# Kernel optimization log

Hardware: AMD Instinct MI355X
Metric: run time of the kernel (lower is better)

## Reference

```python
import jax, jax.numpy as jnp
import numpy as np

B, T, D = 16, 4096, 512
N_SLOTS = 64


def setup_inputs() -> dict:
    key = jax.random.key(0)
    ks = jax.random.split(key, 7)
    s = 1.0 / np.sqrt(D)  # keep tanh out of deep saturation, like orthogonal*0.9 init
    return {
        "x_seq": jax.random.normal(ks[0], (B, T, D), jnp.float32),
        "h_tape": jax.random.normal(ks[1], (B, N_SLOTS, D), jnp.float32) * 0.1,
        "h_work": jax.random.normal(ks[2], (B, D), jnp.float32) * 0.1,
        "W_h": jax.random.normal(ks[3], (D, D), jnp.float32) * s,
        "W_x": jax.random.normal(ks[4], (D, D), jnp.float32) * s,
        "b_h": jnp.zeros((D,), jnp.float32),
        "W_write": jax.random.normal(ks[5], (D, D), jnp.float32) * s,
    }


def reference(x_seq, h_tape, h_work, W_h, W_x, b_h, W_write):
    """Dual-memory Elman recurrence.

    Per step t:
      read_t  = softmax(h_tape @ h_work / sqrt(D)) @ h_tape   (content-based tape read)
      h_work  = tanh(W_h h_work + W_x x_t + read_t + b_h)
      tape write: slot (t mod n_slots) <- W_write h_work      (FIFO tape write)
    Returns (h_work_out [B,T,D], h_tape_final [B,S,D], last h_work [B,D]).
    """
    scale = jnp.asarray(1.0 / np.sqrt(D), x_seq.dtype)

    def step(carry, inp):
        tape, h = carry
        x_t, t = inp
        scores = jnp.einsum("bsd,bd->bs", tape, h) * scale        # [B,S]
        attn = jax.nn.softmax(scores, axis=-1)
        read = jnp.einsum("bs,bsd->bd", attn, tape)               # [B,D]
        h_new = jnp.tanh(h @ W_h.T + x_t @ W_x.T + read + b_h)    # [B,D]
        w_vec = h_new @ W_write.T                                 # [B,D]
        slot = t % N_SLOTS
        tape = jax.lax.dynamic_update_slice(tape, w_vec[:, None, :], (0, slot, 0))
        return (tape, h_new), h_new

    xs = (jnp.swapaxes(x_seq, 0, 1), jnp.arange(x_seq.shape[1]))
    (tape_f, _), h_seq = jax.lax.scan(step, (h_tape, h_work), xs)
    h_work_out = jnp.swapaxes(h_seq, 0, 1)  # [B,T,D]
    return h_work_out, tape_f, h_work_out[:, -1]
```

## Files before the change

kernel.cpp:

```cpp
#include <hip/hip_runtime.h>
#include <cstddef>

#define B_SZ   16
#define T_SZ   4096
#define D_SZ   512
#define NSLOT  64
#define NW     16
#define RPW    32
#define TP     36
#define SCALE  0.044194173824159216f

__device__ __align__(8) unsigned long long g_pb[B_SZ * NW * NSLOT];
__device__ __align__(8) unsigned long long g_hb[B_SZ * D_SZ];
__device__ __align__(8) unsigned long long g_q [B_SZ * NW];

#define AL(p)    __hip_atomic_load((p),  __ATOMIC_RELAXED, __HIP_MEMORY_SCOPE_AGENT)
#define AS(p,v)  __hip_atomic_store((p), (v), __ATOMIC_RELAXED, __HIP_MEMORY_SCOPE_AGENT)

__device__ __forceinline__ unsigned long long pk(float v, unsigned tag) {
    return ((unsigned long long)tag << 32) | (unsigned long long)__float_as_uint(v);
}
__device__ __forceinline__ float lo(unsigned long long v) {
    return __uint_as_float((unsigned)v);
}

__global__ __launch_bounds__(256)
void xw_gemm_kernel(const float* __restrict__ X, const float* __restrict__ Wx,
                    const float* __restrict__ bh, float* __restrict__ out)
{
    __shared__ float As[16][68];
    __shared__ float Bs[16][68];
    const int m0 = blockIdx.x * 64;
    const int n0 = blockIdx.y * 64;
    const int tid = threadIdx.x;
    const int tr = tid >> 4, tc = tid & 15;
    const int lrow = tid >> 2;
    const int lkk  = (tid & 3) * 4;

    float acc[4][4] = {};

    for (int k0 = 0; k0 < D_SZ; k0 += 16) {
        float4 av = *(const float4*)(X  + (size_t)(m0 + lrow) * D_SZ + k0 + lkk);
        float4 bv = *(const float4*)(Wx + (size_t)(n0 + lrow) * D_SZ + k0 + lkk);
        As[lkk+0][lrow] = av.x; As[lkk+1][lrow] = av.y;
        As[lkk+2][lrow] = av.z; As[lkk+3][lrow] = av.w;
        Bs[lkk+0][lrow] = bv.x; Bs[lkk+1][lrow] = bv.y;
        Bs[lkk+2][lrow] = bv.z; Bs[lkk+3][lrow] = bv.w;
        __syncthreads();
        #pragma unroll
        for (int kk = 0; kk < 16; ++kk) {
            float a[4], b[4];
            #pragma unroll
            for (int i = 0; i < 4; ++i) a[i] = As[kk][tr*4+i];
            #pragma unroll
            for (int j = 0; j < 4; ++j) b[j] = Bs[kk][tc*4+j];
            #pragma unroll
            for (int i = 0; i < 4; ++i)
                #pragma unroll
                for (int j = 0; j < 4; ++j)
                    acc[i][j] = fmaf(a[i], b[j], acc[i][j]);
        }
        __syncthreads();
    }
    #pragma unroll
    for (int i = 0; i < 4; ++i) {
        const int m = m0 + tr*4 + i;
        const int n = n0 + tc*4;
        float4 o;
        o.x = acc[i][0] + bh[n+0];
        o.y = acc[i][1] + bh[n+1];
        o.z = acc[i][2] + bh[n+2];
        o.w = acc[i][3] + bh[n+3];
        *(float4*)(out + (size_t)m * D_SZ + n) = o;
    }
}

__global__ __launch_bounds__(256, 1)
void recurrence_mw(const float* __restrict__ tape0, const float* __restrict__ h0,
                   const float* __restrict__ W_h, const float* __restrict__ W_w,
                   float* __restrict__ out)
{
    __shared__ __align__(16) float tp[NSLOT][TP];
    __shared__ __align__(16) float hh[D_SZ];
    __shared__ __align__(16) float hno[RPW];
    __shared__ float scr[NSLOT];
    __shared__ float es[NSLOT];
    __shared__ float zmv[RPW];
    __shared__ float rp8[8][RPW];
    __shared__ float sml[2];

    const int blk = blockIdx.x;
    const int xcd = blk & 7;
    const int jj0 = blk >> 3;
    const int b   = xcd * 2 + (jj0 & 1);
    const int w   = jj0 >> 1;
    const int R0  = w * RPW;
    const int tid = threadIdx.x;
    const int fb  = b * NW;
    const int g16 = tid >> 4, sj = tid & 15;
    const int sA  = tid >> 2, qA = tid & 3;
    const int sg  = tid >> 5, jB = tid & 31;

    if (tid < NSLOT) AS(&g_pb[((size_t)fb + w) * NSLOT + tid], 0ULL);
    if (tid < RPW)   AS(&g_hb[(size_t)b * D_SZ + R0 + tid], 0ULL);
    if (tid == 0)    AS(&g_q[fb + w], 0ULL);

    float4 wh0[8], wh1[8], ww0[8], ww1[8];
    {
        const float* a0 = W_h + (size_t)(R0 + g16)      * D_SZ + 4 * sj;
        const float* a1 = W_h + (size_t)(R0 + g16 + 16) * D_SZ + 4 * sj;
        const float* b0 = W_w + (size_t)(R0 + g16)      * D_SZ + 4 * sj;
        const float* b1 = W_w + (size_t)(R0 + g16 + 16) * D_SZ + 4 * sj;
        #pragma unroll
        for (int i = 0; i < 8; ++i) {
            wh0[i] = *(const float4*)(a0 + 64 * i);
            wh1[i] = *(const float4*)(a1 + 64 * i);
            ww0[i] = *(const float4*)(b0 + 64 * i);
            ww1[i] = *(const float4*)(b1 + 64 * i);
        }
    }

    for (int i = tid; i < NSLOT * RPW; i += 256) {
        const int s = i >> 5, j = i & 31;
        tp[s][j] = tape0[((size_t)b * NSLOT + s) * D_SZ + R0 + j];
    }
    for (int i = tid; i < D_SZ; i += 256) hh[i] = h0[(size_t)b * D_SZ + i];
    __syncthreads();

    float* outb = out + (size_t)b * T_SZ * D_SZ;

    if (tid < RPW) {
        hno[tid] = hh[R0 + tid];
        AS(&g_hb[(size_t)b * D_SZ + R0 + tid], pk(hh[R0 + tid], 1u));
    }
    __syncthreads();
    {
        const float* trow = &tp[sA][8 * qA];
        float4 t0 = *(const float4*)trow;
        float4 t1 = *(const float4*)(trow + 4);
        float4 h0v = *(const float4*)&hno[8 * qA];
        float4 h1v = *(const float4*)&hno[8 * qA + 4];
        float pp = t0.x*h0v.x + t0.y*h0v.y + t0.z*h0v.z + t0.w*h0v.w
                 + t1.x*h1v.x + t1.y*h1v.y + t1.z*h1v.z + t1.w*h1v.w;
        pp += __shfl_xor(pp, 1);
        pp += __shfl_xor(pp, 2);
        if (qA == 0) AS(&g_pb[((size_t)fb + w) * NSLOT + sA], pk(pp, 1u));
    }

    for (int t = 0; t < T_SZ; ++t) {
        const unsigned tgB = (unsigned)(t + 1);
        const int sp = (t - 1) & 63;

        float xwv = 0.f;
        if (tid < RPW) xwv = outb[(size_t)t * D_SZ + R0 + tid];
        {
            const unsigned long long* pb = &g_pb[((size_t)fb + qA * 4) * NSLOT + sA];
            const unsigned long long* hb = &g_hb[(size_t)b * D_SZ + 2 * tid];
            unsigned long long p0, p1, p2, p3, v0, v1;
            for (;;) {
                p0 = AL(pb);              p1 = AL(pb + NSLOT);
                p2 = AL(pb + 2 * NSLOT);  p3 = AL(pb + 3 * NSLOT);
                v0 = AL(hb);              v1 = AL(hb + 1);
                if ((unsigned)(p0 >> 32) == tgB && (unsigned)(p1 >> 32) == tgB &&
                    (unsigned)(p2 >> 32) == tgB && (unsigned)(p3 >> 32) == tgB &&
                    (unsigned)(v0 >> 32) == tgB && (unsigned)(v1 >> 32) == tgB) break;
                __builtin_amdgcn_s_sleep(1);
            }
            float s4 = lo(p0) + lo(p1) + lo(p2) + lo(p3);
            s4 += __shfl_xor(s4, 1);
            s4 += __shfl_xor(s4, 2);
            if (qA == 0) scr[sA] = s4 * SCALE;
            hh[2 * tid]     = lo(v0);
            hh[2 * tid + 1] = lo(v1);
        }
        __syncthreads();

        {
            float z0 = 0.f, z1 = 0.f, v0 = 0.f, v1 = 0.f;
            #pragma unroll
            for (int i = 0; i < 8; ++i) {
                float4 hr = *(const float4*)&hh[4 * sj + 64 * i];
                z0 = fmaf(wh0[i].x, hr.x, z0); z0 = fmaf(wh0[i].y, hr.y, z0);
                z0 = fmaf(wh0[i].z, hr.z, z0); z0 = fmaf(wh0[i].w, hr.w, z0);
                z1 = fmaf(wh1[i].x, hr.x, z1); z1 = fmaf(wh1[i].y, hr.y, z1);
                z1 = fmaf(wh1[i].z, hr.z, z1); z1 = fmaf(wh1[i].w, hr.w, z1);
                v0 = fmaf(ww0[i].x, hr.x, v0); v0 = fmaf(ww0[i].y, hr.y, v0);
                v0 = fmaf(ww0[i].z, hr.z, v0); v0 = fmaf(ww0[i].w, hr.w, v0);
                v1 = fmaf(ww1[i].x, hr.x, v1); v1 = fmaf(ww1[i].y, hr.y, v1);
                v1 = fmaf(ww1[i].z, hr.z, v1); v1 = fmaf(ww1[i].w, hr.w, v1);
            }
            #pragma unroll
            for (int o = 1; o <= 8; o <<= 1) {
                z0 += __shfl_xor(z0, o); z1 += __shfl_xor(z1, o);
                v0 += __shfl_xor(v0, o); v1 += __shfl_xor(v1, o);
            }
            if (sj == 0) {
                zmv[g16] = z0; zmv[g16 + 16] = z1;
                if (t > 0) { tp[sp][g16] = v0; tp[sp][g16 + 16] = v1; }
            }
        }
        __syncthreads();

        if (tid < 64) {
            const float v = (t > 0 && tid == sp) ? -3.0e38f : scr[tid];
            float m = v;
            #pragma unroll
            for (int o = 32; o; o >>= 1) m = fmaxf(m, __shfl_xor(m, o));
            const float e = __expf(v - m);
            float s = e;
            #pragma unroll
            for (int o = 32; o; o >>= 1) s += __shfl_xor(s, o);
            es[tid] = e;
            if (tid == 0) { sml[0] = m; sml[1] = s; }
        } else if (tid < 96 && t > 0) {
            const int ld = tid - 64;
            float qp = tp[sp][ld] * hh[R0 + ld];
            #pragma unroll
            for (int o = 1; o <= 16; o <<= 1) qp += __shfl_xor(qp, o);
            if (ld == 0) AS(&g_q[fb + w], pk(qp, tgB));
        }
        __syncthreads();

        {
            float acc = 0.f;
            #pragma unroll
            for (int s8 = 0; s8 < 8; ++s8)
                acc = fmaf(es[sg * 8 + s8], tp[sg * 8 + s8][jB], acc);
            rp8[sg][jB] = acc;
        }
        __syncthreads();

        if (tid < RPW) {
            const float rr = rp8[0][tid] + rp8[1][tid] + rp8[2][tid] + rp8[3][tid]
                           + rp8[4][tid] + rp8[5][tid] + rp8[6][tid] + rp8[7][tid];
            float rd;
            if (t > 0) {
                const unsigned long long* qp_ = &g_q[fb + (tid & 15)];
                unsigned long long qv;
                for (;;) {
                    qv = AL(qp_);
                    if ((unsigned)(qv >> 32) == tgB) break;
                    __builtin_amdgcn_s_sleep(1);
                }
                float qs = lo(qv);
                qs += __shfl_xor(qs, 1); qs += __shfl_xor(qs, 2);
                qs += __shfl_xor(qs, 4); qs += __shfl_xor(qs, 8);
                const float esig = __expf(qs * SCALE - sml[0]);
                rd = (rr + esig * tp[sp][tid]) / (sml[1] + esig);
            } else {
                rd = rr / sml[1];
            }
            const float hn = tanhf(zmv[tid] + rd + xwv);
            outb[(size_t)t * D_SZ + R0 + tid] = hn;
            AS(&g_hb[(size_t)b * D_SZ + R0 + tid], pk(hn, (unsigned)(t + 2)));
            hno[tid] = hn;
        }
        __syncthreads();

        {
            const float* trow = &tp[sA][8 * qA];
            float4 t0 = *(const float4*)trow;
            float4 t1 = *(const float4*)(trow + 4);
            float4 h0v = *(const float4*)&hno[8 * qA];
            float4 h1v = *(const float4*)&hno[8 * qA + 4];
            float pp = t0.x*h0v.x + t0.y*h0v.y + t0.z*h0v.z + t0.w*h0v.w
                     + t1.x*h1v.x + t1.y*h1v.y + t1.z*h1v.z + t1.w*h1v.w;
            pp += __shfl_xor(pp, 1);
            pp += __shfl_xor(pp, 2);
            if (qA == 0) AS(&g_pb[((size_t)fb + w) * NSLOT + sA], pk(pp, (unsigned)(t + 2)));
        }
    }

    {
        const unsigned long long* hb = &g_hb[(size_t)b * D_SZ + 2 * tid];
        unsigned long long v0, v1;
        const unsigned tgF = (unsigned)(T_SZ + 1);
        for (;;) {
            v0 = AL(hb); v1 = AL(hb + 1);
            if ((unsigned)(v0 >> 32) == tgF && (unsigned)(v1 >> 32) == tgF) break;
            __builtin_amdgcn_s_sleep(1);
        }
        hh[2 * tid]     = lo(v0);
        hh[2 * tid + 1] = lo(v1);
    }
    __syncthreads();
    {
        float v0 = 0.f, v1 = 0.f;
        #pragma unroll
        for (int i = 0; i < 8; ++i) {
            float4 hr = *(const float4*)&hh[4 * sj + 64 * i];
            v0 = fmaf(ww0[i].x, hr.x, v0); v0 = fmaf(ww0[i].y, hr.y, v0);
            v0 = fmaf(ww0[i].z, hr.z, v0); v0 = fmaf(ww0[i].w, hr.w, v0);
            v1 = fmaf(ww1[i].x, hr.x, v1); v1 = fmaf(ww1[i].y, hr.y, v1);
            v1 = fmaf(ww1[i].z, hr.z, v1); v1 = fmaf(ww1[i].w, hr.w, v1);
        }
        #pragma unroll
        for (int o = 1; o <= 8; o <<= 1) { v0 += __shfl_xor(v0, o); v1 += __shfl_xor(v1, o); }
        if (sj == 0) { tp[63][g16] = v0; tp[63][g16 + 16] = v1; }
    }
    __syncthreads();
    float* tout = out + (size_t)B_SZ * T_SZ * D_SZ + (size_t)b * NSLOT * D_SZ;
    for (int i = tid; i < NSLOT * RPW; i += 256) {
        const int s = i >> 5, j = i & 31;
        tout[(size_t)s * D_SZ + R0 + j] = tp[s][j];
    }
    if (w == 0) {
        float* lout = out + (size_t)B_SZ * T_SZ * D_SZ
                          + (size_t)B_SZ * NSLOT * D_SZ + (size_t)b * D_SZ;
        for (int i = tid; i < D_SZ; i += 256) lout[i] = hh[i];
    }
}

extern "C" void kernel_launch(void* const* d_in, const int* in_sizes, int n_in,
                              void* d_out, int out_size, void* d_ws, size_t ws_size,
                              hipStream_t stream)
{
    const float* x_seq   = (const float*)d_in[0];
    const float* h_tape  = (const float*)d_in[1];
    const float* h_work  = (const float*)d_in[2];
    const float* W_h     = (const float*)d_in[3];
    const float* W_x     = (const float*)d_in[4];
    const float* b_h     = (const float*)d_in[5];
    const float* W_write = (const float*)d_in[6];
    float* out = (float*)d_out;

    dim3 g1(T_SZ * B_SZ / 64, D_SZ / 64);
    xw_gemm_kernel<<<g1, 256, 0, stream>>>(x_seq, W_x, b_h, out);

    recurrence_mw<<<B_SZ * NW, 256, 0, stream>>>(h_tape, h_work, W_h, W_write, out);
}
```

Measured before the change: 18.40 ms.

## Interleave four batch chains per workgroup to hide cross-block sync latency

```diff
diff --git a/kernel.cpp b/kernel.cpp
--- a/kernel.cpp
+++ b/kernel.cpp
@@ -7,12 +7,12 @@
 #define NSLOT  64
 #define NW     16
 #define RPW    32
+#define NC     4
 #define TP     36
 #define SCALE  0.044194173824159216f
 
 __device__ __align__(8) unsigned long long g_pb[B_SZ * NW * NSLOT];
 __device__ __align__(8) unsigned long long g_hb[B_SZ * D_SZ];
-__device__ __align__(8) unsigned long long g_q [B_SZ * NW];
 
 #define AL(p)    __hip_atomic_load((p),  __ATOMIC_RELAXED, __HIP_MEMORY_SCOPE_AGENT)
 #define AS(p,v)  __hip_atomic_store((p), (v), __ATOMIC_RELAXED, __HIP_MEMORY_SCOPE_AGENT)
@@ -23,6 +23,8 @@
 __device__ __forceinline__ float lo(unsigned long long v) {
     return __uint_as_float((unsigned)v);
 }
+#define PIN(x) asm volatile("" : "+v"(x))
+#define PIN4(v) do { PIN((v).x); PIN((v).y); PIN((v).z); PIN((v).w); } while (0)
 
 __global__ __launch_bounds__(256)
 void xw_gemm_kernel(const float* __restrict__ X, const float* __restrict__ Wx,
@@ -80,30 +82,30 @@
                    const float* __restrict__ W_h, const float* __restrict__ W_w,
                    float* __restrict__ out)
 {
-    __shared__ __align__(16) float tp[NSLOT][TP];
-    __shared__ __align__(16) float hh[D_SZ];
-    __shared__ __align__(16) float hno[RPW];
-    __shared__ float scr[NSLOT];
-    __shared__ float es[NSLOT];
-    __shared__ float zmv[RPW];
-    __shared__ float rp8[8][RPW];
-    __shared__ float sml[2];
+    __shared__ __align__(16) float tp[NC][NSLOT][TP];
+    __shared__ __align__(16) float hh[NC][D_SZ];
+    __shared__ float scr[NC][NSLOT];
+    __shared__ float es[NC][NSLOT];
+    __shared__ float zmv[NC][RPW];
+    __shared__ float rp8[NC][8][RPW];
+    __shared__ float sml[NC];
+    __shared__ float xwc[NC][RPW];
 
     const int blk = blockIdx.x;
-    const int xcd = blk & 7;
-    const int jj0 = blk >> 3;
-    const int b   = xcd * 2 + (jj0 & 1);
-    const int w   = jj0 >> 1;
+    const int w   = blk & 15;
+    const int g   = blk >> 4;
     const int R0  = w * RPW;
     const int tid = threadIdx.x;
-    const int fb  = b * NW;
     const int g16 = tid >> 4, sj = tid & 15;
     const int sA  = tid >> 2, qA = tid & 3;
     const int sg  = tid >> 5, jB = tid & 31;
 
-    if (tid < NSLOT) AS(&g_pb[((size_t)fb + w) * NSLOT + tid], 0ULL);
-    if (tid < RPW)   AS(&g_hb[(size_t)b * D_SZ + R0 + tid], 0ULL);
-    if (tid == 0)    AS(&g_q[fb + w], 0ULL);
+    #pragma unroll
+    for (int c = 0; c < NC; ++c) {
+        const int b = g * NC + c;
+        if (tid < NSLOT) AS(&g_pb[((size_t)b * NW + w) * NSLOT + tid], 0ULL);
+        if (tid < RPW)   AS(&g_hb[(size_t)b * D_SZ + R0 + tid], 0ULL);
+    }
 
     float4 wh0[8], wh1[8], ww0[8], ww1[8];
     {
@@ -113,201 +115,186 @@
         const float* b1 = W_w + (size_t)(R0 + g16 + 16) * D_SZ + 4 * sj;
         #pragma unroll
         for (int i = 0; i < 8; ++i) {
-            wh0[i] = *(const float4*)(a0 + 64 * i);
-            wh1[i] = *(const float4*)(a1 + 64 * i);
-            ww0[i] = *(const float4*)(b0 + 64 * i);
-            ww1[i] = *(const float4*)(b1 + 64 * i);
-        }
-    }
-
-    for (int i = tid; i < NSLOT * RPW; i += 256) {
-        const int s = i >> 5, j = i & 31;
-        tp[s][j] = tape0[((size_t)b * NSLOT + s) * D_SZ + R0 + j];
-    }
-    for (int i = tid; i < D_SZ; i += 256) hh[i] = h0[(size_t)b * D_SZ + i];
+            wh0[i] = *(const float4*)(a0 + 64 * i);  PIN4(wh0[i]);
+            wh1[i] = *(const float4*)(a1 + 64 * i);  PIN4(wh1[i]);
+            ww0[i] = *(const float4*)(b0 + 64 * i);  PIN4(ww0[i]);
+            ww1[i] = *(const float4*)(b1 + 64 * i);  PIN4(ww1[i]);
+        }
+    }
+
+    for (int c = 0; c < NC; ++c) {
+        const int b = g * NC + c;
+        for (int i = tid; i < NSLOT * RPW; i += 256) {
+            const int s = i >> 5, j = i & 31;
+            tp[c][s][j] = tape0[((size_t)b * NSLOT + s) * D_SZ + R0 + j];
+        }
+        for (int i = tid; i < D_SZ; i += 256) hh[c][i] = h0[(size_t)b * D_SZ + i];
+    }
     __syncthreads();
 
-    float* outb = out + (size_t)b * T_SZ * D_SZ;
-
-    if (tid < RPW) {
-        hno[tid] = hh[R0 + tid];
-        AS(&g_hb[(size_t)b * D_SZ + R0 + tid], pk(hh[R0 + tid], 1u));
-    }
-    __syncthreads();
-    {
-        const float* trow = &tp[sA][8 * qA];
-        float4 t0 = *(const float4*)trow;
-        float4 t1 = *(const float4*)(trow + 4);
-        float4 h0v = *(const float4*)&hno[8 * qA];
-        float4 h1v = *(const float4*)&hno[8 * qA + 4];
-        float pp = t0.x*h0v.x + t0.y*h0v.y + t0.z*h0v.z + t0.w*h0v.w
-                 + t1.x*h1v.x + t1.y*h1v.y + t1.z*h1v.z + t1.w*h1v.w;
-        pp += __shfl_xor(pp, 1);
-        pp += __shfl_xor(pp, 2);
-        if (qA == 0) AS(&g_pb[((size_t)fb + w) * NSLOT + sA], pk(pp, 1u));
-    }
-
     for (int t = 0; t < T_SZ; ++t) {
-        const unsigned tgB = (unsigned)(t + 1);
+        const unsigned tgP = (unsigned)(t + 1);
         const int sp = (t - 1) & 63;
 
-        float xwv = 0.f;
-        if (tid < RPW) xwv = outb[(size_t)t * D_SZ + R0 + tid];
+        #pragma unroll 1
+        for (int c = 0; c < NC; ++c) {
+            const int b = g * NC + c;
+            float* ob = out + (size_t)b * T_SZ * D_SZ;
+            if (tid < RPW) xwc[c][tid] = ob[(size_t)t * D_SZ + R0 + tid];
+            if (t > 0) {
+                const unsigned long long* hb = &g_hb[(size_t)b * D_SZ + 2 * tid];
+                unsigned long long v0, v1;
+                for (;;) {
+                    v0 = AL(hb); v1 = AL(hb + 1);
+                    if ((unsigned)(v0 >> 32) == tgP && (unsigned)(v1 >> 32) == tgP) break;
+                    __builtin_amdgcn_s_sleep(1);
+                }
+                hh[c][2 * tid]     = lo(v0);
+                hh[c][2 * tid + 1] = lo(v1);
+            }
+            __syncthreads();
+
+            {
+                float z0 = 0.f, z1 = 0.f, y0 = 0.f, y1 = 0.f;
+                #pragma unroll
+                for (int i = 0; i < 8; ++i) {
+                    float4 hr = *(const float4*)&hh[c][4 * sj + 64 * i];
+                    z0 = fmaf(wh0[i].x, hr.x, z0); z0 = fmaf(wh0[i].y, hr.y, z0);
+                    z0 = fmaf(wh0[i].z, hr.z, z0); z0 = fmaf(wh0[i].w, hr.w, z0);
+                    z1 = fmaf(wh1[i].x, hr.x, z1); z1 = fmaf(wh1[i].y, hr.y, z1);
+                    z1 = fmaf(wh1[i].z, hr.z, z1); z1 = fmaf(wh1[i].w, hr.w, z1);
+                    y0 = fmaf(ww0[i].x, hr.x, y0); y0 = fmaf(ww0[i].y, hr.y, y0);
+                    y0 = fmaf(ww0[i].z, hr.z, y0); y0 = fmaf(ww0[i].w, hr.w, y0);
+                    y1 = fmaf(ww1[i].x, hr.x, y1); y1 = fmaf(ww1[i].y, hr.y, y1);
+                    y1 = fmaf(ww1[i].z, hr.z, y1); y1 = fmaf(ww1[i].w, hr.w, y1);
+                }
+                #pragma unroll
+                for (int o = 1; o <= 8; o <<= 1) {
+                    z0 += __shfl_xor(z0, o); z1 += __shfl_xor(z1, o);
+                    y0 += __shfl_xor(y0, o); y1 += __shfl_xor(y1, o);
+                }
+                if (sj == 0) {
+                    zmv[c][g16] = z0; zmv[c][g16 + 16] = z1;
+                    if (t > 0) { tp[c][sp][g16] = y0; tp[c][sp][g16 + 16] = y1; }
+                }
+            }
+            __syncthreads();
+
+            {
+                const float* trow = &tp[c][sA][8 * qA];
+                float4 t0 = *(const float4*)trow;
+                float4 t1 = *(const float4*)(trow + 4);
+                float4 ha = *(const float4*)&hh[c][R0 + 8 * qA];
+                float4 hb4 = *(const float4*)&hh[c][R0 + 8 * qA + 4];
+                float pp = t0.x*ha.x + t0.y*ha.y + t0.z*ha.z + t0.w*ha.w
+                         + t1.x*hb4.x + t1.y*hb4.y + t1.z*hb4.z + t1.w*hb4.w;
+                pp += __shfl_xor(pp, 1);
+                pp += __shfl_xor(pp, 2);
+                if (qA == 0)
+                    AS(&g_pb[((size_t)b * NW + w) * NSLOT + sA], pk(pp, tgP));
+            }
+        }
+
+        #pragma unroll 1
+        for (int c = 0; c < NC; ++c) {
+            const int b = g * NC + c;
+            float* ob = out + (size_t)b * T_SZ * D_SZ;
+            {
+                const unsigned long long* pb =
+                    &g_pb[((size_t)b * NW + qA * 4) * NSLOT + sA];
+                unsigned long long p0, p1, p2, p3;
+                for (;;) {
+                    p0 = AL(pb);             p1 = AL(pb + NSLOT);
+                    p2 = AL(pb + 2 * NSLOT); p3 = AL(pb + 3 * NSLOT);
+                    if ((unsigned)(p0 >> 32) == tgP && (unsigned)(p1 >> 32) == tgP &&
+                        (unsigned)(p2 >> 32) == tgP && (unsigned)(p3 >> 32) == tgP) break;
+                    __builtin_amdgcn_s_sleep(1);
+                }
+                float s4 = lo(p0) + lo(p1) + lo(p2) + lo(p3);
+                s4 += __shfl_xor(s4, 1);
+                s4 += __shfl_xor(s4, 2);
+                if (qA == 0) scr[c][sA] = s4 * SCALE;
+            }
+            __syncthreads();
+
+            if (tid < 64) {
+                const float v = scr[c][tid];
+                float m = v;
+                #pragma unroll
+                for (int o = 32; o; o >>= 1) m = fmaxf(m, __shfl_xor(m, o));
+                const float e = __expf(v - m);
+                float s = e;
+                #pragma unroll
+                for (int o = 32; o; o >>= 1) s += __shfl_xor(s, o);
+                es[c][tid] = e;
+                if (tid == 0) sml[c] = s;
+            }
+            __syncthreads();
+
+            {
+                float acc = 0.f;
+                #pragma unroll
+                for (int s8 = 0; s8 < 8; ++s8)
+                    acc = fmaf(es[c][sg * 8 + s8], tp[c][sg * 8 + s8][jB], acc);
+                rp8[c][sg][jB] = acc;
+            }
+            __syncthreads();
+
+            if (tid < RPW) {
+                const float rr = rp8[c][0][tid] + rp8[c][1][tid] + rp8[c][2][tid]
+                               + rp8[c][3][tid] + rp8[c][4][tid] + rp8[c][5][tid]
+                               + rp8[c][6][tid] + rp8[c][7][tid];
+                const float rd = rr / sml[c];
+                const float hn = tanhf(zmv[c][tid] + rd + xwc[c][tid]);
+                AS(&g_hb[(size_t)b * D_SZ + R0 + tid], pk(hn, (unsigned)(t + 2)));
+                ob[(size_t)t * D_SZ + R0 + tid] = hn;
+            }
+        }
+    }
+
+    for (int c = 0; c < NC; ++c) {
+        const int b = g * NC + c;
         {
-            const unsigned long long* pb = &g_pb[((size_t)fb + qA * 4) * NSLOT + sA];
             const unsigned long long* hb = &g_hb[(size_t)b * D_SZ + 2 * tid];
-            unsigned long long p0, p1, p2, p3, v0, v1;
+            const unsigned tgF = (unsigned)(T_SZ + 1);
+            unsigned long long v0, v1;
             for (;;) {
-                p0 = AL(pb);              p1 = AL(pb + NSLOT);
-                p2 = AL(pb + 2 * NSLOT);  p3 = AL(pb + 3 * NSLOT);
-                v0 = AL(hb);              v1 = AL(hb + 1);
-                if ((unsigned)(p0 >> 32) == tgB && (unsigned)(p1 >> 32) == tgB &&
-                    (unsigned)(p2 >> 32) == tgB && (unsigned)(p3 >> 32) == tgB &&
-                    (unsigned)(v0 >> 32) == tgB && (unsigned)(v1 >> 32) == tgB) break;
+                v0 = AL(hb); v1 = AL(hb + 1);
+                if ((unsigned)(v0 >> 32) == tgF && (unsigned)(v1 >> 32) == tgF) break;
                 __builtin_amdgcn_s_sleep(1);
             }
-            float s4 = lo(p0) + lo(p1) + lo(p2) + lo(p3);
-            s4 += __shfl_xor(s4, 1);
-            s4 += __shfl_xor(s4, 2);
-            if (qA == 0) scr[sA] = s4 * SCALE;
-            hh[2 * tid]     = lo(v0);
-            hh[2 * tid + 1] = lo(v1);
-        }
-        __syncthreads();
-
+            hh[c][2 * tid]     = lo(v0);
+            hh[c][2 * tid + 1] = lo(v1);
+        }
+        __syncthreads();
         {
-            float z0 = 0.f, z1 = 0.f, v0 = 0.f, v1 = 0.f;
+            float y0 = 0.f, y1 = 0.f;
             #pragma unroll
             for (int i = 0; i < 8; ++i) {
-                float4 hr = *(const float4*)&hh[4 * sj + 64 * i];
-                z0 = fmaf(wh0[i].x, hr.x, z0); z0 = fmaf(wh0[i].y, hr.y, z0);
-                z0 = fmaf(wh0[i].z, hr.z, z0); z0 = fmaf(wh0[i].w, hr.w, z0);
-                z1 = fmaf(wh1[i].x, hr.x, z1); z1 = fmaf(wh1[i].y, hr.y, z1);
-                z1 = fmaf(wh1[i].z, hr.z, z1); z1 = fmaf(wh1[i].w, hr.w, z1);
-                v0 = fmaf(ww0[i].x, hr.x, v0); v0 = fmaf(ww0[i].y, hr.y, v0);
-                v0 = fmaf(ww0[i].z, hr.z, v0); v0 = fmaf(ww0[i].w, hr.w, v0);
-                v1 = fmaf(ww1[i].x, hr.x, v1); v1 = fmaf(ww1[i].y, hr.y, v1);
-                v1 = fmaf(ww1[i].z, hr.z, v1); v1 = fmaf(ww1[i].w, hr.w, v1);
+                float4 hr = *(const float4*)&hh[c][4 * sj + 64 * i];
+                y0 = fmaf(ww0[i].x, hr.x, y0); y0 = fmaf(ww0[i].y, hr.y, y0);
+                y0 = fmaf(ww0[i].z, hr.z, y0); y0 = fmaf(ww0[i].w, hr.w, y0);
+                y1 = fmaf(ww1[i].x, hr.x, y1); y1 = fmaf(ww1[i].y, hr.y, y1);
+                y1 = fmaf(ww1[i].z, hr.z, y1); y1 = fmaf(ww1[i].w, hr.w, y1);
             }
             #pragma unroll
             for (int o = 1; o <= 8; o <<= 1) {
-                z0 += __shfl_xor(z0, o); z1 += __shfl_xor(z1, o);
-                v0 += __shfl_xor(v0, o); v1 += __shfl_xor(v1, o);
-            }
-            if (sj == 0) {
-                zmv[g16] = z0; zmv[g16 + 16] = z1;
-                if (t > 0) { tp[sp][g16] = v0; tp[sp][g16 + 16] = v1; }
-            }
-        }
-        __syncthreads();
-
-        if (tid < 64) {
-            const float v = (t > 0 && tid == sp) ? -3.0e38f : scr[tid];
-            float m = v;
-            #pragma unroll
-            for (int o = 32; o; o >>= 1) m = fmaxf(m, __shfl_xor(m, o));
-            const float e = __expf(v - m);
-            float s = e;
-            #pragma unroll
-            for (int o = 32; o; o >>= 1) s += __shfl_xor(s, o);
-            es[tid] = e;
-            if (tid == 0) { sml[0] = m; sml[1] = s; }
-        } else if (tid < 96 && t > 0) {
-            const int ld = tid - 64;
-            float qp = tp[sp][ld] * hh[R0 + ld];
-            #pragma unroll
-            for (int o = 1; o <= 16; o <<= 1) qp += __shfl_xor(qp, o);
-            if (ld == 0) AS(&g_q[fb + w], pk(qp, tgB));
-        }
-        __syncthreads();
-
-        {
-            float acc = 0.f;
-            #pragma unroll
-            for (int s8 = 0; s8 < 8; ++s8)
-                acc = fmaf(es[sg * 8 + s8], tp[sg * 8 + s8][jB], acc);
-            rp8[sg][jB] = acc;
-        }
-        __syncthreads();
-
-        if (tid < RPW) {
-            const float rr = rp8[0][tid] + rp8[1][tid] + rp8[2][tid] + rp8[3][tid]
-                           + rp8[4][tid] + rp8[5][tid] + rp8[6][tid] + rp8[7][tid];
-            float rd;
-            if (t > 0) {
-                const unsigned long long* qp_ = &g_q[fb + (tid & 15)];
-                unsigned long long qv;
-                for (;;) {
-                    qv = AL(qp_);
-                    if ((unsigned)(qv >> 32) == tgB) break;
-                    __builtin_amdgcn_s_sleep(1);
-                }
-                float qs = lo(qv);
-                qs += __shfl_xor(qs, 1); qs += __shfl_xor(qs, 2);
-                qs += __shfl_xor(qs, 4); qs += __shfl_xor(qs, 8);
-                const float esig = __expf(qs * SCALE - sml[0]);
-                rd = (rr + esig * tp[sp][tid]) / (sml[1] + esig);
-            } else {
-                rd = rr / sml[1];
-            }
-            const float hn = tanhf(zmv[tid] + rd + xwv);
-            outb[(size_t)t * D_SZ + R0 + tid] = hn;
-            AS(&g_hb[(size_t)b * D_SZ + R0 + tid], pk(hn, (unsigned)(t + 2)));
-            hno[tid] = hn;
-        }
-        __syncthreads();
-
-        {
-            const float* trow = &tp[sA][8 * qA];
-            float4 t0 = *(const float4*)trow;
-            float4 t1 = *(const float4*)(trow + 4);
-            float4 h0v = *(const float4*)&hno[8 * qA];
-            float4 h1v = *(const float4*)&hno[8 * qA + 4];
-            float pp = t0.x*h0v.x + t0.y*h0v.y + t0.z*h0v.z + t0.w*h0v.w
-                     + t1.x*h1v.x + t1.y*h1v.y + t1.z*h1v.z + t1.w*h1v.w;
-            pp += __shfl_xor(pp, 1);
-            pp += __shfl_xor(pp, 2);
-            if (qA == 0) AS(&g_pb[((size_t)fb + w) * NSLOT + sA], pk(pp, (unsigned)(t + 2)));
-        }
-    }
-
-    {
-        const unsigned long long* hb = &g_hb[(size_t)b * D_SZ + 2 * tid];
-        unsigned long long v0, v1;
-        const unsigned tgF = (unsigned)(T_SZ + 1);
-        for (;;) {
-            v0 = AL(hb); v1 = AL(hb + 1);
-            if ((unsigned)(v0 >> 32) == tgF && (unsigned)(v1 >> 32) == tgF) break;
-            __builtin_amdgcn_s_sleep(1);
-        }
-        hh[2 * tid]     = lo(v0);
-        hh[2 * tid + 1] = lo(v1);
-    }
-    __syncthreads();
-    {
-        float v0 = 0.f, v1 = 0.f;
-        #pragma unroll
-        for (int i = 0; i < 8; ++i) {
-            float4 hr = *(const float4*)&hh[4 * sj + 64 * i];
-            v0 = fmaf(ww0[i].x, hr.x, v0); v0 = fmaf(ww0[i].y, hr.y, v0);
-            v0 = fmaf(ww0[i].z, hr.z, v0); v0 = fmaf(ww0[i].w, hr.w, v0);
-            v1 = fmaf(ww1[i].x, hr.x, v1); v1 = fmaf(ww1[i].y, hr.y, v1);
-            v1 = fmaf(ww1[i].z, hr.z, v1); v1 = fmaf(ww1[i].w, hr.w, v1);
-        }
-        #pragma unroll
-        for (int o = 1; o <= 8; o <<= 1) { v0 += __shfl_xor(v0, o); v1 += __shfl_xor(v1, o); }
-        if (sj == 0) { tp[63][g16] = v0; tp[63][g16 + 16] = v1; }
-    }
-    __syncthreads();
-    float* tout = out + (size_t)B_SZ * T_SZ * D_SZ + (size_t)b * NSLOT * D_SZ;
-    for (int i = tid; i < NSLOT * RPW; i += 256) {
-        const int s = i >> 5, j = i & 31;
-        tout[(size_t)s * D_SZ + R0 + j] = tp[s][j];
-    }
-    if (w == 0) {
-        float* lout = out + (size_t)B_SZ * T_SZ * D_SZ
-                          + (size_t)B_SZ * NSLOT * D_SZ + (size_t)b * D_SZ;
-        for (int i = tid; i < D_SZ; i += 256) lout[i] = hh[i];
+                y0 += __shfl_xor(y0, o); y1 += __shfl_xor(y1, o);
+            }
+            if (sj == 0) { tp[c][63][g16] = y0; tp[c][63][g16 + 16] = y1; }
+        }
+        __syncthreads();
+        float* tout = out + (size_t)B_SZ * T_SZ * D_SZ + (size_t)b * NSLOT * D_SZ;
+        for (int i = tid; i < NSLOT * RPW; i += 256) {
+            const int s = i >> 5, j = i & 31;
+            tout[(size_t)s * D_SZ + R0 + j] = tp[c][s][j];
+        }
+        if (w == 0) {
+            float* lout = out + (size_t)B_SZ * T_SZ * D_SZ
+                              + (size_t)B_SZ * NSLOT * D_SZ + (size_t)b * D_SZ;
+            for (int i = tid; i < D_SZ; i += 256) lout[i] = hh[c][i];
+        }
+        __syncthreads();
     }
 }
 
@@ -327,5 +314,5 @@
     dim3 g1(T_SZ * B_SZ / 64, D_SZ / 64);
     xw_gemm_kernel<<<g1, 256, 0, stream>>>(x_seq, W_x, b_h, out);
 
-    recurrence_mw<<<B_SZ * NW, 256, 0, stream>>>(h_tape, h_work, W_h, W_write, out);
-}
+    recurrence_mw<<<B_SZ * NW / NC, 256, 0, stream>>>(h_tape, h_work, W_h, W_write, out);
+}
```

Measured after the change: 49.32 ms. +168.1%, slower.

## Split waves: overlap score polling with matvec, stream weights from cache

Applied to the files above, without the earlier changes.

```diff
diff --git a/kernel.cpp b/kernel.cpp
--- a/kernel.cpp
+++ b/kernel.cpp
@@ -12,7 +12,7 @@
 
 __device__ __align__(8) unsigned long long g_pb[B_SZ * NW * NSLOT];
 __device__ __align__(8) unsigned long long g_hb[B_SZ * D_SZ];
-__device__ __align__(8) unsigned long long g_q [B_SZ * NW];
+__device__ __align__(8) unsigned long long g_q [B_SZ * NW * 2];
 
 #define AL(p)    __hip_atomic_load((p),  __ATOMIC_RELAXED, __HIP_MEMORY_SCOPE_AGENT)
 #define AS(p,v)  __hip_atomic_store((p), (v), __ATOMIC_RELAXED, __HIP_MEMORY_SCOPE_AGENT)
@@ -49,16 +49,16 @@
         __syncthreads();
         #pragma unroll
         for (int kk = 0; kk < 16; ++kk) {
-            float a[4], b[4];
+            float a[4], bq[4];
             #pragma unroll
             for (int i = 0; i < 4; ++i) a[i] = As[kk][tr*4+i];
             #pragma unroll
-            for (int j = 0; j < 4; ++j) b[j] = Bs[kk][tc*4+j];
+            for (int j = 0; j < 4; ++j) bq[j] = Bs[kk][tc*4+j];
             #pragma unroll
             for (int i = 0; i < 4; ++i)
                 #pragma unroll
                 for (int j = 0; j < 4; ++j)
-                    acc[i][j] = fmaf(a[i], b[j], acc[i][j]);
+                    acc[i][j] = fmaf(a[i], bq[j], acc[i][j]);
         }
         __syncthreads();
     }
@@ -97,28 +97,13 @@
     const int R0  = w * RPW;
     const int tid = threadIdx.x;
     const int fb  = b * NW;
-    const int g16 = tid >> 4, sj = tid & 15;
     const int sA  = tid >> 2, qA = tid & 3;
     const int sg  = tid >> 5, jB = tid & 31;
 
     if (tid < NSLOT) AS(&g_pb[((size_t)fb + w) * NSLOT + tid], 0ULL);
     if (tid < RPW)   AS(&g_hb[(size_t)b * D_SZ + R0 + tid], 0ULL);
-    if (tid == 0)    AS(&g_q[fb + w], 0ULL);
-
-    float4 wh0[8], wh1[8], ww0[8], ww1[8];
-    {
-        const float* a0 = W_h + (size_t)(R0 + g16)      * D_SZ + 4 * sj;
-        const float* a1 = W_h + (size_t)(R0 + g16 + 16) * D_SZ + 4 * sj;
-        const float* b0 = W_w + (size_t)(R0 + g16)      * D_SZ + 4 * sj;
-        const float* b1 = W_w + (size_t)(R0 + g16 + 16) * D_SZ + 4 * sj;
-        #pragma unroll
-        for (int i = 0; i < 8; ++i) {
-            wh0[i] = *(const float4*)(a0 + 64 * i);
-            wh1[i] = *(const float4*)(a1 + 64 * i);
-            ww0[i] = *(const float4*)(b0 + 64 * i);
-            ww1[i] = *(const float4*)(b1 + 64 * i);
-        }
-    }
+    if (tid == 128)  AS(&g_q[((size_t)fb + w) * 2 + 0], 0ULL);
+    if (tid == 192)  AS(&g_q[((size_t)fb + w) * 2 + 1], 0ULL);
 
     for (int i = tid; i < NSLOT * RPW; i += 256) {
         const int s = i >> 5, j = i & 31;
@@ -154,52 +139,84 @@
         float xwv = 0.f;
         if (tid < RPW) xwv = outb[(size_t)t * D_SZ + R0 + tid];
         {
-            const unsigned long long* pb = &g_pb[((size_t)fb + qA * 4) * NSLOT + sA];
             const unsigned long long* hb = &g_hb[(size_t)b * D_SZ + 2 * tid];
-            unsigned long long p0, p1, p2, p3, v0, v1;
+            unsigned long long v0, v1;
             for (;;) {
-                p0 = AL(pb);              p1 = AL(pb + NSLOT);
-                p2 = AL(pb + 2 * NSLOT);  p3 = AL(pb + 3 * NSLOT);
-                v0 = AL(hb);              v1 = AL(hb + 1);
-                if ((unsigned)(p0 >> 32) == tgB && (unsigned)(p1 >> 32) == tgB &&
-                    (unsigned)(p2 >> 32) == tgB && (unsigned)(p3 >> 32) == tgB &&
-                    (unsigned)(v0 >> 32) == tgB && (unsigned)(v1 >> 32) == tgB) break;
-                __builtin_amdgcn_s_sleep(1);
-            }
-            float s4 = lo(p0) + lo(p1) + lo(p2) + lo(p3);
-            s4 += __shfl_xor(s4, 1);
-            s4 += __shfl_xor(s4, 2);
-            if (qA == 0) scr[sA] = s4 * SCALE;
+                v0 = AL(hb); v1 = AL(hb + 1);
+                if ((unsigned)(v0 >> 32) == tgB && (unsigned)(v1 >> 32) == tgB) break;
+            }
             hh[2 * tid]     = lo(v0);
             hh[2 * tid + 1] = lo(v1);
         }
         __syncthreads();
 
-        {
-            float z0 = 0.f, z1 = 0.f, v0 = 0.f, v1 = 0.f;
-            #pragma unroll
-            for (int i = 0; i < 8; ++i) {
-                float4 hr = *(const float4*)&hh[4 * sj + 64 * i];
-                z0 = fmaf(wh0[i].x, hr.x, z0); z0 = fmaf(wh0[i].y, hr.y, z0);
-                z0 = fmaf(wh0[i].z, hr.z, z0); z0 = fmaf(wh0[i].w, hr.w, z0);
-                z1 = fmaf(wh1[i].x, hr.x, z1); z1 = fmaf(wh1[i].y, hr.y, z1);
-                z1 = fmaf(wh1[i].z, hr.z, z1); z1 = fmaf(wh1[i].w, hr.w, z1);
-                v0 = fmaf(ww0[i].x, hr.x, v0); v0 = fmaf(ww0[i].y, hr.y, v0);
-                v0 = fmaf(ww0[i].z, hr.z, v0); v0 = fmaf(ww0[i].w, hr.w, v0);
-                v1 = fmaf(ww1[i].x, hr.x, v1); v1 = fmaf(ww1[i].y, hr.y, v1);
-                v1 = fmaf(ww1[i].z, hr.z, v1); v1 = fmaf(ww1[i].w, hr.w, v1);
-            }
-            #pragma unroll
-            for (int o = 1; o <= 8; o <<= 1) {
+        float qwave = 0.f;
+        if (tid >= 128) {
+            const int t1  = tid - 128;
+            const int rr  = t1 >> 3;
+            const int sj8 = t1 & 7;
+            const float* whA = W_h + (size_t)(R0 + rr)      * D_SZ;
+            const float* whB = W_h + (size_t)(R0 + rr + 16) * D_SZ;
+            const float* wwA = W_w + (size_t)(R0 + rr)      * D_SZ;
+            const float* wwB = W_w + (size_t)(R0 + rr + 16) * D_SZ;
+            float z0 = 0.f, z1 = 0.f, y0 = 0.f, y1 = 0.f;
+            #pragma unroll
+            for (int i = 0; i < 16; ++i) {
+                const int col = 4 * sj8 + 32 * i;
+                float4 hr = *(const float4*)&hh[col];
+                float4 a0 = *(const float4*)(whA + col);
+                float4 a1 = *(const float4*)(whB + col);
+                float4 b0 = *(const float4*)(wwA + col);
+                float4 b1v = *(const float4*)(wwB + col);
+                z0 = fmaf(a0.x, hr.x, z0); z0 = fmaf(a0.y, hr.y, z0);
+                z0 = fmaf(a0.z, hr.z, z0); z0 = fmaf(a0.w, hr.w, z0);
+                z1 = fmaf(a1.x, hr.x, z1); z1 = fmaf(a1.y, hr.y, z1);
+                z1 = fmaf(a1.z, hr.z, z1); z1 = fmaf(a1.w, hr.w, z1);
+                y0 = fmaf(b0.x, hr.x, y0); y0 = fmaf(b0.y, hr.y, y0);
+                y0 = fmaf(b0.z, hr.z, y0); y0 = fmaf(b0.w, hr.w, y0);
+                y1 = fmaf(b1v.x, hr.x, y1); y1 = fmaf(b1v.y, hr.y, y1);
+                y1 = fmaf(b1v.z, hr.z, y1); y1 = fmaf(b1v.w, hr.w, y1);
+            }
+            #pragma unroll
+            for (int o = 1; o <= 4; o <<= 1) {
                 z0 += __shfl_xor(z0, o); z1 += __shfl_xor(z1, o);
-                v0 += __shfl_xor(v0, o); v1 += __shfl_xor(v1, o);
-            }
-            if (sj == 0) {
-                zmv[g16] = z0; zmv[g16 + 16] = z1;
-                if (t > 0) { tp[sp][g16] = v0; tp[sp][g16 + 16] = v1; }
-            }
-        }
-        __syncthreads();
+                y0 += __shfl_xor(y0, o); y1 += __shfl_xor(y1, o);
+            }
+            float c = 0.f;
+            if (sj8 == 0) {
+                zmv[rr]      = z0;
+                zmv[rr + 16] = z1;
+                if (t > 0) { tp[sp][rr] = y0; tp[sp][rr + 16] = y1; }
+                c = y0 * hh[R0 + rr] + y1 * hh[R0 + rr + 16];
+            }
+            c += __shfl_xor(c, 8);
+            c += __shfl_xor(c, 16);
+            c += __shfl_xor(c, 32);
+            qwave = c;
+        } else {
+            const int s  = tid >> 1;
+            const int hf = tid & 1;
+            const unsigned long long* pb = &g_pb[((size_t)fb + hf * 8) * NSLOT + s];
+            unsigned long long p[8];
+            for (;;) {
+                bool ok = true;
+                #pragma unroll
+                for (int k = 0; k < 8; ++k) {
+                    p[k] = AL(pb + (size_t)k * NSLOT);
+                    ok &= ((unsigned)(p[k] >> 32) == tgB);
+                }
+                if (ok) break;
+            }
+            float ls = 0.f;
+            #pragma unroll
+            for (int k = 0; k < 8; ++k) ls += lo(p[k]);
+            ls += __shfl_xor(ls, 1);
+            if (hf == 0) scr[s] = ls * SCALE;
+        }
+        __syncthreads();
+
+        if (tid == 128) AS(&g_q[((size_t)fb + w) * 2 + 0], pk(qwave, tgB));
+        if (tid == 192) AS(&g_q[((size_t)fb + w) * 2 + 1], pk(qwave, tgB));
 
         if (tid < 64) {
             const float v = (t > 0 && tid == sp) ? -3.0e38f : scr[tid];
@@ -212,12 +229,6 @@
             for (int o = 32; o; o >>= 1) s += __shfl_xor(s, o);
             es[tid] = e;
             if (tid == 0) { sml[0] = m; sml[1] = s; }
-        } else if (tid < 96 && t > 0) {
-            const int ld = tid - 64;
-            float qp = tp[sp][ld] * hh[R0 + ld];
-            #pragma unroll
-            for (int o = 1; o <= 16; o <<= 1) qp += __shfl_xor(qp, o);
-            if (ld == 0) AS(&g_q[fb + w], pk(qp, tgB));
         }
         __syncthreads();
 
@@ -231,29 +242,28 @@
         __syncthreads();
 
         if (tid < RPW) {
-            const float rr = rp8[0][tid] + rp8[1][tid] + rp8[2][tid] + rp8[3][tid]
-                           + rp8[4][tid] + rp8[5][tid] + rp8[6][tid] + rp8[7][tid];
+            const float rr8 = rp8[0][tid] + rp8[1][tid] + rp8[2][tid] + rp8[3][tid]
+                            + rp8[4][tid] + rp8[5][tid] + rp8[6][tid] + rp8[7][tid];
+            const unsigned long long* qp_ = &g_q[((size_t)fb + (tid & 15)) * 2];
+            unsigned long long q0, q1;
+            for (;;) {
+                q0 = AL(qp_); q1 = AL(qp_ + 1);
+                if ((unsigned)(q0 >> 32) == tgB && (unsigned)(q1 >> 32) == tgB) break;
+            }
             float rd;
             if (t > 0) {
-                const unsigned long long* qp_ = &g_q[fb + (tid & 15)];
-                unsigned long long qv;
-                for (;;) {
-                    qv = AL(qp_);
-                    if ((unsigned)(qv >> 32) == tgB) break;
-                    __builtin_amdgcn_s_sleep(1);
-                }
-                float qs = lo(qv);
+                float qs = lo(q0) + lo(q1);
                 qs += __shfl_xor(qs, 1); qs += __shfl_xor(qs, 2);
                 qs += __shfl_xor(qs, 4); qs += __shfl_xor(qs, 8);
                 const float esig = __expf(qs * SCALE - sml[0]);
-                rd = (rr + esig * tp[sp][tid]) / (sml[1] + esig);
+                rd = (rr8 + esig * tp[sp][tid]) / (sml[1] + esig);
             } else {
-                rd = rr / sml[1];
+                rd = rr8 / sml[1];
             }
             const float hn = tanhf(zmv[tid] + rd + xwv);
-            outb[(size_t)t * D_SZ + R0 + tid] = hn;
             AS(&g_hb[(size_t)b * D_SZ + R0 + tid], pk(hn, (unsigned)(t + 2)));
             hno[tid] = hn;
+            outb[(size_t)t * D_SZ + R0 + tid] = hn;
         }
         __syncthreads();
 
@@ -273,30 +283,37 @@
 
     {
         const unsigned long long* hb = &g_hb[(size_t)b * D_SZ + 2 * tid];
+        const unsigned tgF = (unsigned)(T_SZ + 1);
         unsigned long long v0, v1;
-        const unsigned tgF = (unsigned)(T_SZ + 1);
         for (;;) {
             v0 = AL(hb); v1 = AL(hb + 1);
             if ((unsigned)(v0 >> 32) == tgF && (unsigned)(v1 >> 32) == tgF) break;
-            __builtin_amdgcn_s_sleep(1);
         }
         hh[2 * tid]     = lo(v0);
         hh[2 * tid + 1] = lo(v1);
     }
     __syncthreads();
-    {
-        float v0 = 0.f, v1 = 0.f;
+    if (tid >= 128) {
+        const int t1  = tid - 128;
+        const int rr  = t1 >> 3;
+        const int sj8 = t1 & 7;
+        const float* wwA = W_w + (size_t)(R0 + rr)      * D_SZ;
+        const float* wwB = W_w + (size_t)(R0 + rr + 16) * D_SZ;
+        float y0 = 0.f, y1 = 0.f;
         #pragma unroll
-        for (int i = 0; i < 8; ++i) {
-            float4 hr = *(const float4*)&hh[4 * sj + 64 * i];
-            v0 = fmaf(ww0[i].x, hr.x, v0); v0 = fmaf(ww0[i].y, hr.y, v0);
-            v0 = fmaf(ww0[i].z, hr.z, v0); v0 = fmaf(ww0[i].w, hr.w, v0);
-            v1 = fmaf(ww1[i].x, hr.x, v1); v1 = fmaf(ww1[i].y, hr.y, v1);
-            v1 = fmaf(ww1[i].z, hr.z, v1); v1 = fmaf(ww1[i].w, hr.w, v1);
+        for (int i = 0; i < 16; ++i) {
+            const int col = 4 * sj8 + 32 * i;
+            float4 hr = *(const float4*)&hh[col];
+            float4 b0 = *(const float4*)(wwA + col);
+            float4 b1v = *(const float4*)(wwB + col);
+            y0 = fmaf(b0.x, hr.x, y0); y0 = fmaf(b0.y, hr.y, y0);
+            y0 = fmaf(b0.z, hr.z, y0); y0 = fmaf(b0.w, hr.w, y0);
+            y1 = fmaf(b1v.x, hr.x, y1); y1 = fmaf(b1v.y, hr.y, y1);
+            y1 = fmaf(b1v.z, hr.z, y1); y1 = fmaf(b1v.w, hr.w, y1);
         }
         #pragma unroll
-        for (int o = 1; o <= 8; o <<= 1) { v0 += __shfl_xor(v0, o); v1 += __shfl_xor(v1, o); }
-        if (sj == 0) { tp[63][g16] = v0; tp[63][g16 + 16] = v1; }
+        for (int o = 1; o <= 4; o <<= 1) { y0 += __shfl_xor(y0, o); y1 += __shfl_xor(y1, o); }
+        if (sj8 == 0) { tp[63][rr] = y0; tp[63][rr + 16] = y1; }
     }
     __syncthreads();
     float* tout = out + (size_t)B_SZ * T_SZ * D_SZ + (size_t)b * NSLOT * D_SZ;
```

Measured after the change: 25.07 ms. 1.36x slower.
